# Kernel optimization log

Hardware: AMD Instinct MI355X
Metric: run time of the kernel (lower is better)

The kernel has to match this reference:

```python
import jax, jax.numpy as jnp
import numpy as np

B, T, V, H, L = 128, 512, 96, 512, 3  # batch, seq_len, n_tokens, n_hidden, n_layers


def setup_inputs() -> dict:
    key = jax.random.key(0)
    ks = jax.random.split(key, 16)
    k = 1.0 / np.sqrt(H)  # PyTorch LSTM/Linear uniform init bound

    def u(kk, shape):
        return jax.random.uniform(kk, shape, jnp.float32, -k, k)

    return {
        "x": jax.random.normal(ks[0], (B, T, V), jnp.float32),
        "h0": jnp.zeros((L, B, H), jnp.float32),
        "c0": jnp.zeros((L, B, H), jnp.float32),
        # layer 0 (input dim V), layers 1-2 (input dim H); gate order i,f,g,o
        "W_ih0": u(ks[1], (4 * H, V)), "W_hh0": u(ks[2], (4 * H, H)),
        "b_ih0": u(ks[3], (4 * H,)), "b_hh0": u(ks[4], (4 * H,)),
        "W_ih1": u(ks[5], (4 * H, H)), "W_hh1": u(ks[6], (4 * H, H)),
        "b_ih1": u(ks[7], (4 * H,)), "b_hh1": u(ks[8], (4 * H,)),
        "W_ih2": u(ks[9], (4 * H, H)), "W_hh2": u(ks[10], (4 * H, H)),
        "b_ih2": u(ks[11], (4 * H,)), "b_hh2": u(ks[12], (4 * H,)),
        "W_fc": u(ks[13], (V, H)), "b_fc": u(ks[14], (V,)),
    }


def _lstm_layer(x, h0, c0, W_ih, W_hh, b_ih, b_hh):
    # Precompute input-to-gate GEMM for the whole sequence: [B,T,4H]
    xg = jnp.einsum('btd,gd->btg', x, W_ih) + b_ih + b_hh

    def step(carry, xg_t):
        h, c = carry
        g = xg_t + h @ W_hh.T  # [B,4H]
        i, f, gg, o = jnp.split(g, 4, axis=-1)
        c = jax.nn.sigmoid(f) * c + jax.nn.sigmoid(i) * jnp.tanh(gg)
        h = jax.nn.sigmoid(o) * jnp.tanh(c)
        return (h, c), h

    (hT, cT), ys = jax.lax.scan(step, (h0, c0), jnp.swapaxes(xg, 0, 1))
    return jnp.swapaxes(ys, 0, 1), hT, cT  # [B,T,H], [B,H], [B,H]


def reference(x, h0, c0, W_ih0, W_hh0, b_ih0, b_hh0, W_ih1, W_hh1, b_ih1, b_hh1,
              W_ih2, W_hh2, b_ih2, b_hh2, W_fc, b_fc):
    params = [(W_ih0, W_hh0, b_ih0, b_hh0),
              (W_ih1, W_hh1, b_ih1, b_hh1),
              (W_ih2, W_hh2, b_ih2, b_hh2)]
    out = x
    hs, cs = [], []
    for l, (Wi, Wh, bi, bh) in enumerate(params):
        out, hT, cT = _lstm_layer(out, h0[l], c0[l], Wi, Wh, bi, bh)
        hs.append(hT)
        cs.append(cT)
    # dropout (inter-layer and post-LSTM) is identity in eval/deterministic mode
    logits = jnp.einsum('bth,vh->btv', out, W_fc) + b_fc  # [B,T,V]
    return logits.reshape(-1, V), jnp.stack(hs), jnp.stack(cs)
```

## Files before the change

### kernel.cpp

```cpp
#include <hip/hip_runtime.h>

#define Bb 128
#define Tt 512
#define Vv 96
#define Hh 512
#define G4v 2048
#define NBLK 194
#define NTHR 512
#define NSTEP 518
#define OUT_H 6291456
#define OUT_C 6488064

typedef _Float16 f16x4 __attribute__((ext_vector_type(4)));
typedef _Float16 f16x8 __attribute__((ext_vector_type(8)));
typedef float f32x4 __attribute__((ext_vector_type(4)));

struct KP {
  const float *x, *h0, *c0;
  const float *Wih0, *Whh0, *bih0, *bhh0;
  const float *Wih1, *Whh1, *bih1, *bhh1;
  const float *Wih2, *Whh2, *bih2, *bhh2;
  const float *Wfc, *bfc;
  float* out;
  unsigned* bar;
  float* fbias;
  _Float16* wimg;
  float* xg;
  _Float16* xb;
  _Float16* ring;
  float* cbuf;
};

__device__ __forceinline__ float sigf(float x) { return 1.f / (1.f + __expf(-x)); }

__device__ __forceinline__ float ld_dc_f32(const float* p) {
  unsigned u = __hip_atomic_load((const unsigned*)p, __ATOMIC_RELAXED, __HIP_MEMORY_SCOPE_AGENT);
  return __uint_as_float(u);
}
__device__ __forceinline__ void st_dc_f32(float* p, float v) {
  __hip_atomic_store((unsigned*)p, __float_as_uint(v), __ATOMIC_RELAXED, __HIP_MEMORY_SCOPE_AGENT);
}
__device__ __forceinline__ f16x4 ld_dc_f16x4(const _Float16* p) {
  unsigned long long u = __hip_atomic_load((const unsigned long long*)p, __ATOMIC_RELAXED, __HIP_MEMORY_SCOPE_AGENT);
  union { unsigned long long u; f16x4 f; } c; c.u = u; return c.f;
}
__device__ __forceinline__ void st_dc_u32(unsigned* p, unsigned v) {
  __hip_atomic_store(p, v, __ATOMIC_RELAXED, __HIP_MEMORY_SCOPE_AGENT);
}

__device__ __forceinline__ void gbar(unsigned* bar, unsigned target) {
  __syncthreads();
  if (threadIdx.x == 0) {
    const unsigned g = (unsigned)blockIdx.x >> 5;
    const unsigned gcnt = (g == 6u) ? (NBLK - 6 * 32) : 32u;
    unsigned p = __hip_atomic_fetch_add(&bar[64 + g * 32], 1u, __ATOMIC_RELAXED, __HIP_MEMORY_SCOPE_AGENT);
    if (p == target * gcnt - 1u) {
      unsigned rp = __hip_atomic_fetch_add(&bar[32], 1u, __ATOMIC_RELAXED, __HIP_MEMORY_SCOPE_AGENT);
      if (rp == target * 7u - 1u) {
        __hip_atomic_store(&bar[0], target, __ATOMIC_RELAXED, __HIP_MEMORY_SCOPE_AGENT);
      } else {
        goto spin;
      }
    } else {
    spin:
      int guard = 0;
      while (__hip_atomic_load(&bar[0], __ATOMIC_RELAXED, __HIP_MEMORY_SCOPE_AGENT) < target) {
        if (++guard > 2000000) break;
        __builtin_amdgcn_s_sleep(1);
      }
    }
  }
  __syncthreads();
  asm volatile("" ::: "memory");
}

template <int KSTEPS, int LSTRIDE, bool SWZ, int NF, bool DC>
__device__ __forceinline__ void gemm1(const _Float16* __restrict__ Abase, int astride,
                                      const _Float16* lds, f32x4 (&acc)[NF]) {
  const int lane = threadIdx.x & 63;
  const int w = threadIdx.x >> 6;
  const int l15 = lane & 15, l4 = lane >> 4;
  const _Float16* ap = Abase + (w * 16 + l15) * astride + l4 * 4;
#pragma unroll
  for (int kb = 0; kb < (KSTEPS + 7) / 8; ++kb) {
    f16x4 av[8];
#pragma unroll
    for (int i = 0; i < 8; ++i) {
      if (kb * 8 + i < KSTEPS) {
        const _Float16* p = ap + (kb * 8 + i) * 16;
        av[i] = DC ? ld_dc_f16x4(p) : *(const f16x4*)p;
      }
    }
#pragma unroll
    for (int i = 0; i < 8; ++i) {
      if (kb * 8 + i < KSTEPS) {
        const int kk = (kb * 8 + i) * 16;
#pragma unroll
        for (int n = 0; n < NF; ++n) {
          const int r = n * 16 + l15;
          int idx = r * LSTRIDE + kk + l4 * 4;
          if (SWZ) idx ^= (r & 7) << 3;
          f16x4 bv = *(const f16x4*)(lds + idx);
          acc[n] = __builtin_amdgcn_mfma_f32_16x16x16f16(av[i], bv, acc[n], 0, 0, 0);
        }
      }
    }
  }
}

__global__ __launch_bounds__(256) void prologue_kernel(KP A) {
  const int tid = threadIdx.x, bid = blockIdx.x;
  const int gt = bid * 256 + tid, gn = NBLK * 256;
  for (int i = gt; i < Bb * Tt * Vv; i += gn) A.xb[i] = (_Float16)A.x[i];
  for (int i = gt; i < 3 * Bb * Hh; i += gn) {
    int l = i >> 16, rem = i & 65535;
    A.ring[(l * 4 + 3) * (Bb * Hh) + rem] = (_Float16)A.h0[i];
    A.cbuf[i] = A.c0[i];
  }
  for (int i = gt; i < 3 * G4v; i += gn) {
    int l = i >> 11, c = i & 2047;
    const float* bi = (l == 0) ? A.bih0 : (l == 1) ? A.bih1 : A.bih2;
    const float* bh = (l == 0) ? A.bhh0 : (l == 1) ? A.bhh1 : A.bhh2;
    A.fbias[i] = bi[c] + bh[c];
  }
  for (int i = gt; i < Vv; i += gn) A.fbias[3 * G4v + i] = A.bfc[i];

  _Float16* img = A.wimg + bid * 32768;
  if (bid < 96) {
    int rl = bid / 32, nt = bid % 32;
    const float* Wi = (rl == 0) ? A.Wih0 : (rl == 1) ? A.Wih1 : A.Wih2;
    const int K = (rl == 0) ? Vv : Hh;
    for (int e = tid; e < 64 * K; e += 256) {
      int r = e / K, k = e - r * K;
      float v = Wi[(nt * 64 + r) * K + k];
      int idx = (rl == 0) ? (r * 104 + k) : ((r * 512 + k) ^ ((r & 7) << 3));
      img[idx] = (_Float16)v;
    }
  } else if (bid < 192) {
    int rl = (bid - 96) / 32, j0 = ((bid - 96) % 32) * 16;
    const float* Wh = (rl == 0) ? A.Whh0 : (rl == 1) ? A.Whh1 : A.Whh2;
    for (int e = tid; e < 64 * 512; e += 256) {
      int r = e >> 9, k = e & 511;
      float v = Wh[((r >> 4) * 512 + j0 + (r & 15)) * Hh + k];
      img[(r * 512 + k) ^ ((r & 7) << 3)] = (_Float16)v;
    }
  } else {
    int nt = bid - 192;
    for (int e = tid; e < 48 * 512; e += 256) {
      int r = e >> 9, k = e & 511;
      img[(r * 512 + k) ^ ((r & 7) << 3)] = (_Float16)A.Wfc[(nt * 48 + r) * Hh + k];
    }
  }
}

__global__ __launch_bounds__(NTHR) void lstm_persist(KP A) {
  __shared__ _Float16 wlds[32768];
  const int tid = threadIdx.x, bid = blockIdx.x;
  const int lane = tid & 63, w = tid >> 6;
  const int l15 = lane & 15, l4 = lane >> 4;

  int role, rl = 0, nt = 0, j0 = 0;
  if (bid < 96)       { role = 0; rl = bid / 32; nt = bid % 32; }
  else if (bid < 192) { role = 1; rl = (bid - 96) / 32; j0 = ((bid - 96) % 32) * 16; }
  else                { role = 2; nt = bid - 192; }

  {
    const f16x8* src = (const f16x8*)(A.wimg + bid * 32768);
    f16x8* dst = (f16x8*)wlds;
    for (int e = tid; e < 4096; e += NTHR) dst[e] = src[e];
  }

  float biasr[4] = {0.f, 0.f, 0.f, 0.f};
  float creg[4] = {0.f, 0.f, 0.f, 0.f};
  if (role == 0) {
#pragma unroll
    for (int n = 0; n < 4; ++n) biasr[n] = A.fbias[rl * G4v + nt * 64 + n * 16 + l15];
  } else if (role == 1) {
    const int j = j0 + l15;
#pragma unroll
    for (int q = 0; q < 4; ++q) creg[q] = A.cbuf[rl * (Bb * Hh) + (w * 16 + l4 * 4 + q) * Hh + j];
  } else {
#pragma unroll
    for (int n = 0; n < 3; ++n) biasr[n] = A.fbias[3 * G4v + nt * 48 + n * 16 + l15];
  }
  __syncthreads();

  for (int s = 0; s < NSTEP; ++s) {
    if (role == 0) {
      const int t = s - 2 * rl;
      if (t >= 0 && t < Tt) {
        f32x4 acc[4] = {};
        if (rl == 0) gemm1<6, 104, false, 4, false>(A.xb + t * Vv, Tt * Vv, wlds, acc);
        else         gemm1<32, 512, true, 4, true>(A.ring + ((rl - 1) * 4 + (t & 3)) * (Bb * Hh), Hh, wlds, acc);
        float* xgp = A.xg + (rl * 4 + (t & 3)) * (Bb * G4v) + nt * 64;
#pragma unroll
        for (int n = 0; n < 4; ++n)
#pragma unroll
          for (int q = 0; q < 4; ++q) {
            int b = w * 16 + l4 * 4 + q;
            st_dc_f32(xgp + b * G4v + n * 16 + l15, acc[n][q] + biasr[n]);
          }
      }
    } else if (role == 1) {
      const int t = s - 2 * rl - 1;
      if (t >= 0 && t < Tt) {
        const float* xgp = A.xg + (rl * 4 + (t & 3)) * (Bb * G4v);
        const int j = j0 + l15;
        float xr[4][4];
#pragma unroll
        for (int g2 = 0; g2 < 4; ++g2)
#pragma unroll
          for (int q = 0; q < 4; ++q) {
            int b = w * 16 + l4 * 4 + q;
            xr[g2][q] = ld_dc_f32(xgp + b * G4v + g2 * Hh + j);
          }
        f32x4 acc[4] = {};
        gemm1<32, 512, true, 4, true>(A.ring + (rl * 4 + ((t - 1) & 3)) * (Bb * Hh), Hh, wlds, acc);
        _Float16* rp = A.ring + (rl * 4 + (t & 3)) * (Bb * Hh);
#pragma unroll
        for (int q = 0; q < 4; ++q) {
          const int b = w * 16 + l4 * 4 + q;
          float gi = acc[0][q] + xr[0][q];
          float gf = acc[1][q] + xr[1][q];
          float gg = acc[2][q] + xr[2][q];
          float go = acc[3][q] + xr[3][q];
          float iv = sigf(gi), fv = sigf(gf), gv = tanhf(gg), ov = sigf(go);
          float cn = fv * creg[q] + iv * gv;
          creg[q] = cn;
          float hv = ov * tanhf(cn);
          union { _Float16 h; unsigned short u; } cv; cv.h = (_Float16)hv;
          unsigned hb = cv.u;
          unsigned ob = (unsigned)__shfl_xor((int)hb, 1, 64);
          if ((l15 & 1) == 0) {
            st_dc_u32((unsigned*)(rp + b * Hh + j), hb | (ob << 16));
          }
          if (t == Tt - 1) {
            A.out[OUT_H + (rl * Bb + b) * Hh + j] = hv;
            A.out[OUT_C + (rl * Bb + b) * Hh + j] = cn;
          }
        }
      }
    } else {
      const int t = s - 6;
      if (t >= 0 && t < Tt) {
        f32x4 acc[3] = {};
        gemm1<32, 512, true, 3, true>(A.ring + (8 + (t & 3)) * (Bb * Hh), Hh, wlds, acc);
#pragma unroll
        for (int n = 0; n < 3; ++n)
#pragma unroll
          for (int q = 0; q < 4; ++q) {
            int b = w * 16 + l4 * 4 + q;
            A.out[(b * Tt + t) * Vv + nt * 48 + n * 16 + l15] = acc[n][q] + biasr[n];
          }
      }
    }
    gbar(A.bar, (unsigned)(s + 1));
  }
}

extern "C" void kernel_launch(void* const* d_in, const int* in_sizes, int n_in,
                              void* d_out, int out_size, void* d_ws, size_t ws_size,
                              hipStream_t stream) {
  char* base = (char*)d_ws;
  KP a;
  a.x    = (const float*)d_in[0];
  a.h0   = (const float*)d_in[1];
  a.c0   = (const float*)d_in[2];
  a.Wih0 = (const float*)d_in[3];  a.Whh0 = (const float*)d_in[4];
  a.bih0 = (const float*)d_in[5];  a.bhh0 = (const float*)d_in[6];
  a.Wih1 = (const float*)d_in[7];  a.Whh1 = (const float*)d_in[8];
  a.bih1 = (const float*)d_in[9];  a.bhh1 = (const float*)d_in[10];
  a.Wih2 = (const float*)d_in[11]; a.Whh2 = (const float*)d_in[12];
  a.bih2 = (const float*)d_in[13]; a.bhh2 = (const float*)d_in[14];
  a.Wfc  = (const float*)d_in[15]; a.bfc  = (const float*)d_in[16];
  a.out  = (float*)d_out;
  a.bar   = (unsigned*)base;
  a.fbias = (float*)(base + 2048);
  a.wimg  = (_Float16*)(base + 27648);
  a.xg    = (float*)(base + 12741632);
  a.xb    = (_Float16*)(base + 25324544);
  a.ring  = (_Float16*)(base + 37907456);
  a.cbuf  = (float*)(base + 39480320);

  hipMemsetAsync(a.bar, 0, 2048, stream);
  hipLaunchKernelGGL(prologue_kernel, dim3(NBLK), dim3(256), 0, stream, a);
  hipLaunchKernelGGL(lstm_persist, dim3(NBLK), dim3(NTHR), 0, stream, a);
}
```

Before: 5.766 ms.

## Fuse input and recurrent GEMMs per block and replace grid barrier with dataflow counters

Each layer block now holds both its W_ih and W_hh slices in LDS (128KB) and computes the input and recurrent GEMMs together, so the xg round-trip through global memory and the separate input-GEMM role go away. The global all-block barrier per step is replaced by per-layer progress counters: each block waits only on the previous layer, its own layer and a bounded lag from downstream consumers, with an 8-deep h ring. This cuts the block count from 194 to 98 and lets layers pipeline as a wavefront. The cost is more serial GEMM work per block on the critical path, and the spin-waits rely on relaxed atomics with a guard timeout.

```diff
diff --git a/kernel.cpp b/kernel.cpp
--- a/kernel.cpp
+++ b/kernel.cpp
@@ -4,10 +4,6 @@
 #define Tt 512
 #define Vv 96
 #define Hh 512
-#define G4v 2048
-#define NBLK 194
-#define NTHR 512
-#define NSTEP 518
 #define OUT_H 6291456
 #define OUT_C 6488064
 
@@ -25,21 +21,12 @@
   unsigned* bar;
   float* fbias;
   _Float16* wimg;
-  float* xg;
   _Float16* xb;
-  _Float16* ring;
-  float* cbuf;
+  _Float16* hring;
 };
 
 __device__ __forceinline__ float sigf(float x) { return 1.f / (1.f + __expf(-x)); }
 
-__device__ __forceinline__ float ld_dc_f32(const float* p) {
-  unsigned u = __hip_atomic_load((const unsigned*)p, __ATOMIC_RELAXED, __HIP_MEMORY_SCOPE_AGENT);
-  return __uint_as_float(u);
-}
-__device__ __forceinline__ void st_dc_f32(float* p, float v) {
-  __hip_atomic_store((unsigned*)p, __float_as_uint(v), __ATOMIC_RELAXED, __HIP_MEMORY_SCOPE_AGENT);
-}
 __device__ __forceinline__ f16x4 ld_dc_f16x4(const _Float16* p) {
   unsigned long long u = __hip_atomic_load((const unsigned long long*)p, __ATOMIC_RELAXED, __HIP_MEMORY_SCOPE_AGENT);
   union { unsigned long long u; f16x4 f; } c; c.u = u; return c.f;
@@ -47,31 +34,12 @@
 __device__ __forceinline__ void st_dc_u32(unsigned* p, unsigned v) {
   __hip_atomic_store(p, v, __ATOMIC_RELAXED, __HIP_MEMORY_SCOPE_AGENT);
 }
-
-__device__ __forceinline__ void gbar(unsigned* bar, unsigned target) {
-  __syncthreads();
-  if (threadIdx.x == 0) {
-    const unsigned g = (unsigned)blockIdx.x >> 5;
-    const unsigned gcnt = (g == 6u) ? (NBLK - 6 * 32) : 32u;
-    unsigned p = __hip_atomic_fetch_add(&bar[64 + g * 32], 1u, __ATOMIC_RELAXED, __HIP_MEMORY_SCOPE_AGENT);
-    if (p == target * gcnt - 1u) {
-      unsigned rp = __hip_atomic_fetch_add(&bar[32], 1u, __ATOMIC_RELAXED, __HIP_MEMORY_SCOPE_AGENT);
-      if (rp == target * 7u - 1u) {
-        __hip_atomic_store(&bar[0], target, __ATOMIC_RELAXED, __HIP_MEMORY_SCOPE_AGENT);
-      } else {
-        goto spin;
-      }
-    } else {
-    spin:
-      int guard = 0;
-      while (__hip_atomic_load(&bar[0], __ATOMIC_RELAXED, __HIP_MEMORY_SCOPE_AGENT) < target) {
-        if (++guard > 2000000) break;
-        __builtin_amdgcn_s_sleep(1);
-      }
-    }
-  }
-  __syncthreads();
-  asm volatile("" ::: "memory");
+__device__ __forceinline__ void wait_ge(unsigned* p, unsigned v) {
+  int guard = 0;
+  while (__hip_atomic_load(p, __ATOMIC_RELAXED, __HIP_MEMORY_SCOPE_AGENT) < v) {
+    if (++guard > 200000) break;
+    __builtin_amdgcn_s_sleep(1);
+  }
 }
 
 template <int KSTEPS, int LSTRIDE, bool SWZ, int NF, bool DC>
@@ -85,14 +53,13 @@
   for (int kb = 0; kb < (KSTEPS + 7) / 8; ++kb) {
     f16x4 av[8];
 #pragma unroll
-    for (int i = 0; i < 8; ++i) {
+    for (int i = 0; i < 8; ++i)
       if (kb * 8 + i < KSTEPS) {
         const _Float16* p = ap + (kb * 8 + i) * 16;
         av[i] = DC ? ld_dc_f16x4(p) : *(const f16x4*)p;
       }
-    }
-#pragma unroll
-    for (int i = 0; i < 8; ++i) {
+#pragma unroll
+    for (int i = 0; i < 8; ++i)
       if (kb * 8 + i < KSTEPS) {
         const int kk = (kb * 8 + i) * 16;
 #pragma unroll
@@ -104,48 +71,89 @@
           acc[n] = __builtin_amdgcn_mfma_f32_16x16x16f16(av[i], bv, acc[n], 0, 0, 0);
         }
       }
+  }
+}
+
+template <int NF>
+__device__ __forceinline__ void gemm2(const _Float16* __restrict__ A1,
+                                      const _Float16* __restrict__ A2,
+                                      const _Float16* lds1, const _Float16* lds2,
+                                      f32x4 (&acc)[NF]) {
+  const int lane = threadIdx.x & 63;
+  const int w = threadIdx.x >> 6;
+  const int l15 = lane & 15, l4 = lane >> 4;
+  const _Float16* ap1 = A1 + (w * 16 + l15) * 512 + l4 * 4;
+  const _Float16* ap2 = A2 + (w * 16 + l15) * 512 + l4 * 4;
+#pragma unroll
+  for (int kb = 0; kb < 4; ++kb) {
+    f16x4 av1[8], av2[8];
+#pragma unroll
+    for (int i = 0; i < 8; ++i) av1[i] = ld_dc_f16x4(ap1 + (kb * 8 + i) * 16);
+#pragma unroll
+    for (int i = 0; i < 8; ++i) av2[i] = ld_dc_f16x4(ap2 + (kb * 8 + i) * 16);
+#pragma unroll
+    for (int i = 0; i < 8; ++i) {
+      const int kk = (kb * 8 + i) * 16;
+#pragma unroll
+      for (int n = 0; n < NF; ++n) {
+        const int r = n * 16 + l15;
+        int idx = (r * 512 + kk + l4 * 4) ^ ((r & 7) << 3);
+        f16x4 b1 = *(const f16x4*)(lds1 + idx);
+        acc[n] = __builtin_amdgcn_mfma_f32_16x16x16f16(av1[i], b1, acc[n], 0, 0, 0);
+      }
+    }
+#pragma unroll
+    for (int i = 0; i < 8; ++i) {
+      const int kk = (kb * 8 + i) * 16;
+#pragma unroll
+      for (int n = 0; n < NF; ++n) {
+        const int r = n * 16 + l15;
+        int idx = (r * 512 + kk + l4 * 4) ^ ((r & 7) << 3);
+        f16x4 b2 = *(const f16x4*)(lds2 + idx);
+        acc[n] = __builtin_amdgcn_mfma_f32_16x16x16f16(av2[i], b2, acc[n], 0, 0, 0);
+      }
     }
   }
 }
 
 __global__ __launch_bounds__(256) void prologue_kernel(KP A) {
   const int tid = threadIdx.x, bid = blockIdx.x;
-  const int gt = bid * 256 + tid, gn = NBLK * 256;
+  const int gt = bid * 256 + tid, gn = 98 * 256;
   for (int i = gt; i < Bb * Tt * Vv; i += gn) A.xb[i] = (_Float16)A.x[i];
   for (int i = gt; i < 3 * Bb * Hh; i += gn) {
     int l = i >> 16, rem = i & 65535;
-    A.ring[(l * 4 + 3) * (Bb * Hh) + rem] = (_Float16)A.h0[i];
-    A.cbuf[i] = A.c0[i];
-  }
-  for (int i = gt; i < 3 * G4v; i += gn) {
+    A.hring[(l * 8 + 7) * (Bb * Hh) + rem] = (_Float16)A.h0[i];
+  }
+  for (int i = gt; i < 3 * 2048; i += gn) {
     int l = i >> 11, c = i & 2047;
     const float* bi = (l == 0) ? A.bih0 : (l == 1) ? A.bih1 : A.bih2;
     const float* bh = (l == 0) ? A.bhh0 : (l == 1) ? A.bhh1 : A.bhh2;
     A.fbias[i] = bi[c] + bh[c];
   }
-  for (int i = gt; i < Vv; i += gn) A.fbias[3 * G4v + i] = A.bfc[i];
-
-  _Float16* img = A.wimg + bid * 32768;
+  for (int i = gt; i < Vv; i += gn) A.fbias[3 * 2048 + i] = A.bfc[i];
+
+  _Float16* img = A.wimg + (size_t)bid * 65536;
   if (bid < 96) {
-    int rl = bid / 32, nt = bid % 32;
-    const float* Wi = (rl == 0) ? A.Wih0 : (rl == 1) ? A.Wih1 : A.Wih2;
-    const int K = (rl == 0) ? Vv : Hh;
-    for (int e = tid; e < 64 * K; e += 256) {
-      int r = e / K, k = e - r * K;
-      float v = Wi[(nt * 64 + r) * K + k];
-      int idx = (rl == 0) ? (r * 104 + k) : ((r * 512 + k) ^ ((r & 7) << 3));
-      img[idx] = (_Float16)v;
-    }
-  } else if (bid < 192) {
-    int rl = (bid - 96) / 32, j0 = ((bid - 96) % 32) * 16;
-    const float* Wh = (rl == 0) ? A.Whh0 : (rl == 1) ? A.Whh1 : A.Whh2;
+    const int l = bid >> 5, j0 = (bid & 31) * 16;
+    const float* Wh = (l == 0) ? A.Whh0 : (l == 1) ? A.Whh1 : A.Whh2;
     for (int e = tid; e < 64 * 512; e += 256) {
       int r = e >> 9, k = e & 511;
-      float v = Wh[((r >> 4) * 512 + j0 + (r & 15)) * Hh + k];
-      img[(r * 512 + k) ^ ((r & 7) << 3)] = (_Float16)v;
+      img[(r * 512 + k) ^ ((r & 7) << 3)] = (_Float16)Wh[((r >> 4) * 512 + j0 + (r & 15)) * Hh + k];
+    }
+    if (l == 0) {
+      for (int e = tid; e < 64 * 96; e += 256) {
+        int r = e / 96, k = e - r * 96;
+        img[32768 + r * 104 + k] = (_Float16)A.Wih0[((r >> 4) * 512 + j0 + (r & 15)) * Vv + k];
+      }
+    } else {
+      const float* Wi = (l == 1) ? A.Wih1 : A.Wih2;
+      for (int e = tid; e < 64 * 512; e += 256) {
+        int r = e >> 9, k = e & 511;
+        img[32768 + ((r * 512 + k) ^ ((r & 7) << 3))] = (_Float16)Wi[((r >> 4) * 512 + j0 + (r & 15)) * Hh + k];
+      }
     }
   } else {
-    int nt = bid - 192;
+    const int nt = bid - 96;
     for (int e = tid; e < 48 * 512; e += 256) {
       int r = e >> 9, k = e & 511;
       img[(r * 512 + k) ^ ((r & 7) << 3)] = (_Float16)A.Wfc[(nt * 48 + r) * Hh + k];
@@ -153,108 +161,101 @@
   }
 }
 
-__global__ __launch_bounds__(NTHR) void lstm_persist(KP A) {
-  __shared__ _Float16 wlds[32768];
+__global__ __launch_bounds__(512) void lstm_persist(KP A) {
+  __shared__ _Float16 wlds[65536];
   const int tid = threadIdx.x, bid = blockIdx.x;
   const int lane = tid & 63, w = tid >> 6;
   const int l15 = lane & 15, l4 = lane >> 4;
-
-  int role, rl = 0, nt = 0, j0 = 0;
-  if (bid < 96)       { role = 0; rl = bid / 32; nt = bid % 32; }
-  else if (bid < 192) { role = 1; rl = (bid - 96) / 32; j0 = ((bid - 96) % 32) * 16; }
-  else                { role = 2; nt = bid - 192; }
+  unsigned* gc = A.bar;
+
+  const bool isfc = (bid >= 96);
+  const int l = isfc ? 2 : (bid >> 5);
+  const int j0 = isfc ? 0 : (bid & 31) * 16;
+  const int nt = isfc ? bid - 96 : 0;
 
   {
-    const f16x8* src = (const f16x8*)(A.wimg + bid * 32768);
+    const f16x8* src = (const f16x8*)(A.wimg + (size_t)bid * 65536);
     f16x8* dst = (f16x8*)wlds;
-    for (int e = tid; e < 4096; e += NTHR) dst[e] = src[e];
-  }
-
-  float biasr[4] = {0.f, 0.f, 0.f, 0.f};
-  float creg[4] = {0.f, 0.f, 0.f, 0.f};
-  if (role == 0) {
-#pragma unroll
-    for (int n = 0; n < 4; ++n) biasr[n] = A.fbias[rl * G4v + nt * 64 + n * 16 + l15];
-  } else if (role == 1) {
-    const int j = j0 + l15;
-#pragma unroll
-    for (int q = 0; q < 4; ++q) creg[q] = A.cbuf[rl * (Bb * Hh) + (w * 16 + l4 * 4 + q) * Hh + j];
+    const int cnt = isfc ? 3072 : 8192;
+    for (int e = tid; e < cnt; e += 512) dst[e] = src[e];
+  }
+
+  if (!isfc) {
+    float biasr[4], creg[4];
+#pragma unroll
+    for (int n = 0; n < 4; ++n) biasr[n] = A.fbias[l * 2048 + n * 512 + j0 + l15];
+#pragma unroll
+    for (int q = 0; q < 4; ++q)
+      creg[q] = A.c0[l * (Bb * Hh) + (w * 16 + l4 * 4 + q) * Hh + j0 + l15];
+    __syncthreads();
+
+    for (int t = 0; t < Tt; ++t) {
+      if (tid == 0) {
+        if (l > 0) wait_ge(&gc[(l - 1) * 32], 32u * (unsigned)(t + 1));
+        if (t > 0) wait_ge(&gc[l * 32], 32u * (unsigned)t);
+        if (t >= 8) {
+          if (l < 2) wait_ge(&gc[(l + 1) * 32], 32u * (unsigned)(t - 7));
+          else       wait_ge(&gc[96], 2u * (unsigned)(t - 7));
+        }
+      }
+      __syncthreads();
+
+      f32x4 acc[4] = {};
+      const _Float16* hprev = A.hring + (size_t)(l * 8 + ((t - 1) & 7)) * (Bb * Hh);
+      if (l == 0) {
+        gemm1<6, 104, false, 4, false>(A.xb + t * Vv, Tt * Vv, wlds + 32768, acc);
+        gemm1<32, 512, true, 4, true>(hprev, Hh, wlds, acc);
+      } else {
+        const _Float16* hin = A.hring + (size_t)((l - 1) * 8 + (t & 7)) * (Bb * Hh);
+        gemm2<4>(hin, hprev, wlds + 32768, wlds, acc);
+      }
+
+      _Float16* rp = A.hring + (size_t)(l * 8 + (t & 7)) * (Bb * Hh);
+      const int j = j0 + l15;
+#pragma unroll
+      for (int q = 0; q < 4; ++q) {
+        const int b = w * 16 + l4 * 4 + q;
+        float gi = acc[0][q] + biasr[0];
+        float gf = acc[1][q] + biasr[1];
+        float gg = acc[2][q] + biasr[2];
+        float go = acc[3][q] + biasr[3];
+        float iv = sigf(gi), fv = sigf(gf), gv = tanhf(gg), ov = sigf(go);
+        float cn = fv * creg[q] + iv * gv;
+        creg[q] = cn;
+        float hv = ov * tanhf(cn);
+        union { _Float16 h; unsigned short u; } cv; cv.h = (_Float16)hv;
+        unsigned hb = cv.u;
+        unsigned ob = (unsigned)__shfl_xor((int)hb, 1, 64);
+        if ((l15 & 1) == 0) st_dc_u32((unsigned*)(rp + b * Hh + j), hb | (ob << 16));
+        if (t == Tt - 1) {
+          A.out[OUT_H + (l * Bb + b) * Hh + j] = hv;
+          A.out[OUT_C + (l * Bb + b) * Hh + j] = cn;
+        }
+      }
+      __syncthreads();
+      if (tid == 0) __hip_atomic_fetch_add(&gc[l * 32], 1u, __ATOMIC_RELAXED, __HIP_MEMORY_SCOPE_AGENT);
+    }
   } else {
-#pragma unroll
-    for (int n = 0; n < 3; ++n) biasr[n] = A.fbias[3 * G4v + nt * 48 + n * 16 + l15];
-  }
-  __syncthreads();
-
-  for (int s = 0; s < NSTEP; ++s) {
-    if (role == 0) {
-      const int t = s - 2 * rl;
-      if (t >= 0 && t < Tt) {
-        f32x4 acc[4] = {};
-        if (rl == 0) gemm1<6, 104, false, 4, false>(A.xb + t * Vv, Tt * Vv, wlds, acc);
-        else         gemm1<32, 512, true, 4, true>(A.ring + ((rl - 1) * 4 + (t & 3)) * (Bb * Hh), Hh, wlds, acc);
-        float* xgp = A.xg + (rl * 4 + (t & 3)) * (Bb * G4v) + nt * 64;
-#pragma unroll
-        for (int n = 0; n < 4; ++n)
-#pragma unroll
-          for (int q = 0; q < 4; ++q) {
-            int b = w * 16 + l4 * 4 + q;
-            st_dc_f32(xgp + b * G4v + n * 16 + l15, acc[n][q] + biasr[n]);
-          }
-      }
-    } else if (role == 1) {
-      const int t = s - 2 * rl - 1;
-      if (t >= 0 && t < Tt) {
-        const float* xgp = A.xg + (rl * 4 + (t & 3)) * (Bb * G4v);
-        const int j = j0 + l15;
-        float xr[4][4];
-#pragma unroll
-        for (int g2 = 0; g2 < 4; ++g2)
-#pragma unroll
-          for (int q = 0; q < 4; ++q) {
-            int b = w * 16 + l4 * 4 + q;
-            xr[g2][q] = ld_dc_f32(xgp + b * G4v + g2 * Hh + j);
-          }
-        f32x4 acc[4] = {};
-        gemm1<32, 512, true, 4, true>(A.ring + (rl * 4 + ((t - 1) & 3)) * (Bb * Hh), Hh, wlds, acc);
-        _Float16* rp = A.ring + (rl * 4 + (t & 3)) * (Bb * Hh);
+    float biasr[3];
+#pragma unroll
+    for (int n = 0; n < 3; ++n) biasr[n] = A.fbias[3 * 2048 + nt * 48 + n * 16 + l15];
+    __syncthreads();
+
+    for (int t = 0; t < Tt; ++t) {
+      if (tid == 0) wait_ge(&gc[64], 32u * (unsigned)(t + 1));
+      __syncthreads();
+      f32x4 acc[3] = {};
+      gemm1<32, 512, true, 3, true>(A.hring + (size_t)(16 + (t & 7)) * (Bb * Hh), Hh, wlds, acc);
+#pragma unroll
+      for (int n = 0; n < 3; ++n)
 #pragma unroll
         for (int q = 0; q < 4; ++q) {
-          const int b = w * 16 + l4 * 4 + q;
-          float gi = acc[0][q] + xr[0][q];
-          float gf = acc[1][q] + xr[1][q];
-          float gg = acc[2][q] + xr[2][q];
-          float go = acc[3][q] + xr[3][q];
-          float iv = sigf(gi), fv = sigf(gf), gv = tanhf(gg), ov = sigf(go);
-          float cn = fv * creg[q] + iv * gv;
-          creg[q] = cn;
-          float hv = ov * tanhf(cn);
-          union { _Float16 h; unsigned short u; } cv; cv.h = (_Float16)hv;
-          unsigned hb = cv.u;
-          unsigned ob = (unsigned)__shfl_xor((int)hb, 1, 64);
-          if ((l15 & 1) == 0) {
-            st_dc_u32((unsigned*)(rp + b * Hh + j), hb | (ob << 16));
-          }
-          if (t == Tt - 1) {
-            A.out[OUT_H + (rl * Bb + b) * Hh + j] = hv;
-            A.out[OUT_C + (rl * Bb + b) * Hh + j] = cn;
-          }
-        }
-      }
-    } else {
-      const int t = s - 6;
-      if (t >= 0 && t < Tt) {
-        f32x4 acc[3] = {};
-        gemm1<32, 512, true, 3, true>(A.ring + (8 + (t & 3)) * (Bb * Hh), Hh, wlds, acc);
-#pragma unroll
-        for (int n = 0; n < 3; ++n)
-#pragma unroll
-          for (int q = 0; q < 4; ++q) {
-            int b = w * 16 + l4 * 4 + q;
-            A.out[(b * Tt + t) * Vv + nt * 48 + n * 16 + l15] = acc[n][q] + biasr[n];
-          }
-      }
-    }
-    gbar(A.bar, (unsigned)(s + 1));
+          int b = w * 16 + l4 * 4 + q;
+          A.out[(b * Tt + t) * Vv + nt * 48 + n * 16 + l15] = acc[n][q] + biasr[n];
+        }
+      __syncthreads();
+      if (tid == 0) __hip_atomic_fetch_add(&gc[96], 1u, __ATOMIC_RELAXED, __HIP_MEMORY_SCOPE_AGENT);
+    }
   }
 }
 
@@ -275,14 +276,12 @@
   a.Wfc  = (const float*)d_in[15]; a.bfc  = (const float*)d_in[16];
   a.out  = (float*)d_out;
   a.bar   = (unsigned*)base;
-  a.fbias = (float*)(base + 2048);
+  a.fbias = (float*)(base + 1024);
   a.wimg  = (_Float16*)(base + 27648);
-  a.xg    = (float*)(base + 12741632);
-  a.xb    = (_Float16*)(base + 25324544);
-  a.ring  = (_Float16*)(base + 37907456);
-  a.cbuf  = (float*)(base + 39480320);
-
-  hipMemsetAsync(a.bar, 0, 2048, stream);
-  hipLaunchKernelGGL(prologue_kernel, dim3(NBLK), dim3(256), 0, stream, a);
-  hipLaunchKernelGGL(lstm_persist, dim3(NBLK), dim3(NTHR), 0, stream, a);
-}
+  a.xb    = (_Float16*)(base + 12872704);
+  a.hring = (_Float16*)(base + 25455616);
+
+  hipMemsetAsync(a.bar, 0, 1024, stream);
+  hipLaunchKernelGGL(prologue_kernel, dim3(98), dim3(256), 0, stream, a);
+  hipLaunchKernelGGL(lstm_persist, dim3(98), dim3(512), 0, stream, a);
+}
```

After: 10.16 ms. 1.76x slower.
